# Kernel optimization log

Measured on AMD Instinct MI355X. Metric: run time of the kernel, lower is better.

## Reference

```python
import jax, jax.numpy as jnp
import numpy as np

# dims (see shape_source): seq S = d_t+1 must equal d_k for the unary quantum loader
B, T, D_IN = 128, 127, 48
DK = 128
S = T + 1            # tokens incl. class token; S == DK
H, L = 8, 6
P = (S * S - S) // 2  # RBS angles per head (pyramid circuit over S wires)


def _pyramid_pairs(n):
    # deterministic pyramid ordering of n(n-1)/2 adjacent-pair Givens rotations
    a, b = [], []
    for k in range(n - 1):
        for i in range(k, -1, -1):
            a.append(i)
            b.append(i + 1)
    return np.asarray(a, np.int32), np.asarray(b, np.int32)


def _build_W(phi, pa, pb, n):
    # classical simulation of the RBS pyramid circuit restricted to the unary
    # subspace: product of Givens rotations -> orthogonal n x n matrix
    def step(W, inp):
        ia, ib, th = inp
        c, s = jnp.cos(th), jnp.sin(th)
        ra, rb = W[ia], W[ib]
        W = W.at[ia].set(c * ra - s * rb)
        W = W.at[ib].set(s * ra + c * rb)
        return W, None
    W0 = jnp.eye(n, dtype=phi.dtype)
    W, _ = jax.lax.scan(step, W0, (pa, pb, phi))
    return W


def _layer_norm(x, g, b, eps=1e-5):
    m = jnp.mean(x, axis=-1, keepdims=True)
    v = jnp.mean((x - m) ** 2, axis=-1, keepdims=True)
    return (x - m) * jax.lax.rsqrt(v + eps) * g + b


def setup_inputs() -> dict:
    key = jax.random.key(0)
    ks = jax.random.split(key, 8)
    f32 = jnp.float32
    return {
        "x": jax.random.normal(ks[0], (B, T, D_IN), f32),
        "embed_w": jax.random.normal(ks[1], (DK, D_IN), f32) / np.sqrt(D_IN),
        "embed_b": jnp.zeros((DK,), f32),
        "class_token": jax.random.normal(ks[2], (DK,), f32) / DK,
        "norm0_g": jnp.ones((DK,), f32),
        "norm0_b": jnp.zeros((DK,), f32),
        "Vw": jax.random.normal(ks[3], (L, H, DK, DK), f32) / np.sqrt(DK),
        "Vb": jnp.zeros((L, H, DK), f32),
        "ln_g": jnp.ones((L, H, DK), f32),
        "ln_b": jnp.zeros((L, H, DK), f32),
        "phi": jax.random.normal(ks[4], (L, H, P), f32) / np.sqrt(S),
        "merger_w": jax.random.normal(ks[5], (L, H), f32) / np.sqrt(H),
        "merger_b": jnp.zeros((L,), f32),
    }


def reference(x, embed_w, embed_b, class_token, norm0_g, norm0_b,
              Vw, Vb, ln_g, ln_b, phi, merger_w, merger_b):
    Bsz = x.shape[0]
    pa, pb = _pyramid_pairs(S)
    # orthogonal score matrices for every (layer, head)
    Ws = jax.vmap(lambda p: _build_W(p, pa, pb, S))(phi.reshape(L * H, P))
    Ws = Ws.reshape(L, H, S, S)

    # embed patches, prepend class token (pos_embedding add is a no-op in the
    # original source: bare `+self.pos_embedding` statement, so it is omitted)
    tok = jnp.einsum('btf,df->btd', x, embed_w) + embed_b
    h = jnp.concatenate([jnp.broadcast_to(class_token, (Bsz, 1, DK)), tok], axis=1)
    h = _layer_norm(h, norm0_g, norm0_b)

    scale = 1.0 / np.sqrt(DK)
    for l in range(L):
        nrm = jnp.sqrt(jnp.sum(h * h, axis=-1))      # input3: token norms [B,S]
        u = h / nrm[..., None]                        # unit tokens (convert_array)
        hh, nn, uu = h, nrm, u

        def head(W, vw, vb, g, be):
            V = jnp.einsum('bsd,ed->bse', hh, vw) + vb
            M = jnp.einsum('bsd,de,bte->bst', uu, W, uu)
            A = (M * M) * (nn[:, :, None] * nn[:, None, :])
            Pm = jax.nn.softmax(A * scale, axis=-1)
            return _layer_norm(jnp.einsum('bst,btd->bsd', Pm, V) + hh, g, be)

        hs = jax.vmap(head)(Ws[l], Vw[l], Vb[l], ln_g[l], ln_b[l])  # [H,B,S,D]
        h = jnp.einsum('hbsd,h->bsd', hs, merger_w[l]) + merger_b[l]
    return h[:, -1, :]
```

## Files before the change

### kernel.cpp

```cpp
#include <hip/hip_runtime.h>
#include <hip/hip_bf16.h>


typedef __bf16 bf16x8 __attribute__((ext_vector_type(8)));
typedef float  f32x4  __attribute__((ext_vector_type(4)));
typedef unsigned int u32;
typedef u32 u32x4 __attribute__((ext_vector_type(4)));
typedef u32 u32x2 __attribute__((ext_vector_type(2)));
typedef unsigned short u16;

__device__ __forceinline__ int sidx(int row, int col)
{
    return row * 128 + ((((col >> 3) ^ (row & 15)) << 3) | (col & 7));
}

__device__ __forceinline__ void gll16(const void* g, void* l)
{
    __builtin_amdgcn_global_load_lds(
        (const __attribute__((address_space(1))) void*)g,
        (__attribute__((address_space(3))) void*)l, 16, 0, 0);
}

__global__ void __launch_bounds__(256)
prep_kernel(const float* __restrict__ phi, float2* __restrict__ csn,
            const float* __restrict__ vw,  __bf16* __restrict__ cvwf)
{
    if (blockIdx.x < 3072) {
        const int mat = blockIdx.x >> 6;
        const int t   = ((blockIdx.x & 63) << 2) + (threadIdx.x >> 6);
        const int j   = threadIdx.x & 63;
        float th = 0.f;
        if (t < 253) {
            const int p = t & 1, i = 2 * j + p;
            const int lim = min(t, 252 - t);
            if (i <= lim) {
                const int k = (t + i) >> 1;
                th = phi[mat * 8128 + ((k * (k + 1)) >> 1) + (k - i)];
            }
        }
        float sn, cs;
        __sincosf(th, &sn, &cs);
        csn[(mat * 256 + t) * 64 + j] = make_float2(cs, sn);
    } else {
        const int f    = (blockIdx.x - 3072) * 256 + threadIdx.x;
        const int lane = f & 63;
        const int k0   = (f >> 6) & 3;
        const int t    = (f >> 8) & 7;
        const int lh   = f >> 11;
        const int row  = t * 16 + (lane & 15);
        const int col  = k0 * 32 + (lane >> 4) * 8;
        const float* src = vw + (lh * 128 + row) * 128 + col;
        __bf16* dst = cvwf + f * 8;
#pragma unroll
        for (int j2 = 0; j2 < 8; j2++) dst[j2] = (__bf16)src[j2];
    }
}

__global__ void __launch_bounds__(64)
build_w_kernel(const float2* __restrict__ csn, __bf16* __restrict__ wt)
{
    const int mat = blockIdx.x >> 7;
    const int c0  = blockIdx.x & 127;
    const int lam = threadIdx.x;

    const float2* base = csn + (mat * 256) * 64 + lam;

    float vlo = (2 * lam     == c0) ? 1.f : 0.f;
    float vhi = (2 * lam + 1 == c0) ? 1.f : 0.f;

    float2 buf[3][16];
#pragma unroll
    for (int k = 0; k < 16; k++) buf[0][k] = base[k * 64];
#pragma unroll
    for (int k = 0; k < 16; k++) buf[1][k] = base[(16 + k) * 64];

#pragma unroll
    for (int g = 0; g < 16; g++) {
        const int cb = g % 3;
        if (g < 14) {
            const int nb = (g + 2) % 3;
#pragma unroll
            for (int k = 0; k < 16; k++)
                buf[nb][k] = base[((g + 2) * 16 + k) * 64];
        }
#pragma unroll
        for (int p = 0; p < 8; p++) {
            {
                const float cs = buf[cb][2 * p].x, sn = buf[cb][2 * p].y;
                float lo = vlo, hi = vhi;
                vlo = cs * lo - sn * hi;
                vhi = sn * lo + cs * hi;
            }
            {
                const float cs = buf[cb][2 * p + 1].x, sn = buf[cb][2 * p + 1].y;
                float y  = __shfl_down(vlo, 1);
                float x  = vhi;
                float xn = cs * x - sn * y;
                float yn = sn * x + cs * y;
                vhi = xn;
                float z = __shfl_up(yn, 1);
                if (lam > 0) vlo = z;
            }
        }
    }

    const int t    = c0 >> 4;
    const int k0w  = lam >> 4;
    const int quad = (lam >> 2) & 3;
    __bf16 va = (__bf16)vlo;
    __bf16 vb = (__bf16)vhi;
    u32 pk = (u32)__builtin_bit_cast(unsigned short, va)
           | ((u32)__builtin_bit_cast(unsigned short, vb) << 16);
    const int frag = (t * 4 + k0w) * 64 + quad * 16 + (c0 & 15);
    ((u32*)wt)[mat * 8192 + frag * 4 + (lam & 3)] = pk;
}

__global__ void __launch_bounds__(512)
embed_kernel(const float* __restrict__ x,  const float* __restrict__ ew,
             const float* __restrict__ eb, const float* __restrict__ ct,
             const float* __restrict__ g0, const float* __restrict__ b0,
             float* __restrict__ hf, __bf16* __restrict__ hb,
             float* __restrict__ invn)
{
    __shared__ float sx[4][48];
    __shared__ float sred[4][2];
    const int d  = threadIdx.x & 127, sq = threadIdx.x >> 7;
    const int wh = (threadIdx.x >> 6) & 1;
    const int b  = blockIdx.x & 127;
    const int s  = (blockIdx.x >> 7) * 4 + sq;

    if (s > 0 && d < 48) sx[sq][d] = x[(b * 127 + (s - 1)) * 48 + d];
    __syncthreads();

    float val;
    if (s == 0) {
        val = ct[d];
    } else {
        float aa = 0.f;
#pragma unroll
        for (int f = 0; f < 48; f++) aa = fmaf(sx[sq][f], ew[d * 48 + f], aa);
        val = aa + eb[d];
    }
    float v = val;
#pragma unroll
    for (int m = 32; m; m >>= 1) v += __shfl_xor(v, m);
    if ((threadIdx.x & 63) == 0) sred[sq][wh] = v;
    __syncthreads();
    float mean = (sred[sq][0] + sred[sq][1]) * (1.f / 128.f);
    float xc   = val - mean;
    __syncthreads();
    v = xc * xc;
#pragma unroll
    for (int m = 32; m; m >>= 1) v += __shfl_xor(v, m);
    if ((threadIdx.x & 63) == 0) sred[sq][wh] = v;
    __syncthreads();
    float var = (sred[sq][0] + sred[sq][1]) * (1.f / 128.f);
    float y   = xc * rsqrtf(var + 1e-5f) * g0[d] + b0[d];
    __syncthreads();
    v = y * y;
#pragma unroll
    for (int m = 32; m; m >>= 1) v += __shfl_xor(v, m);
    if ((threadIdx.x & 63) == 0) sred[sq][wh] = v;
    __syncthreads();
    float ss = sred[sq][0] + sred[sq][1];

    const int o = (b * 128 + s) * 128 + d;
    hf[o] = y;
    hb[o] = (__bf16)y;
    if (d == 0) invn[b * 128 + s] = rsqrtf(ss);
}

__global__ void __launch_bounds__(512, 4)
attn_kernel(int l, int last,
            const float*  __restrict__ hf,  const __bf16* __restrict__ hb,
            const float*  __restrict__ invn, const __bf16* __restrict__ wt,
            const __bf16* __restrict__ vwf, const float* __restrict__ vb,
            const float* __restrict__ lng,  const float* __restrict__ lnb,
            const float* __restrict__ mwp,  __bf16* __restrict__ hs)
{
    __shared__ __align__(16) __bf16 sH[128 * 128];
    __shared__ __align__(16) __bf16 sY[128 * 128];
    __shared__ float sInv[128];
    __shared__ float sVb[128];
    __shared__ float sLg[128];
    __shared__ float sLb[128];

    const int tid  = threadIdx.x;
    const int lane = tid & 63, w = tid >> 6;
    const int l15  = lane & 15, quad = lane >> 4;
    const int b    = blockIdx.x & 127;
    const int hh   = blockIdx.x >> 7;
    const int lh   = l * 8 + hh;

    const __bf16* hbp   = hb  + b * 16384;
    const __bf16* wbase = wt  + (size_t)lh * 16384;
    const __bf16* vbase = vwf + (size_t)lh * 16384;

#pragma unroll
    for (int c = 0; c < 4; c++) {
        const int ch  = tid + c * 512;
        const int row = ch >> 4, cc = ch & 15;
        const int sc  = cc ^ (row & 15);
        gll16(hbp + (row * 16 + sc) * 8, &sH[(c * 512 + w * 64) * 8]);
    }
    if (tid < 128) {
        sInv[tid] = invn[b * 128 + tid];
        sVb[tid]  = vb[lh * 128 + tid];
        sLg[tid]  = lng[lh * 128 + tid];
        sLb[tid]  = lnb[lh * 128 + tid];
    }
    __syncthreads();

    const int r0 = w * 16;
    const int kq = quad * 8;
    const int q4 = quad * 4;
    const f32x4 vzero = {0.f, 0.f, 0.f, 0.f};
    const bool active = !last || (w == 7);

    f32x4 acc[8];

    auto mmGA = [&](const __bf16* gB) {
#pragma unroll
        for (int t = 0; t < 8; t++) acc[t] = vzero;
        __builtin_amdgcn_s_setprio(1);
#pragma unroll
        for (int k0c = 0; k0c < 4; k0c++) {
            bf16x8 a0 = *(const bf16x8*)(&sH[sidx(r0 + l15, k0c * 32 + kq)]);
#pragma unroll
            for (int t = 0; t < 8; t++) {
                bf16x8 bb = *(const bf16x8*)(gB + ((t * 4 + k0c) * 64 + lane) * 8);
                acc[t] = __builtin_amdgcn_mfma_f32_16x16x32_bf16(a0, bb, acc[t], 0, 0, 0);
            }
        }
        __builtin_amdgcn_s_setprio(0);
    };

    auto mmLL = [&](const __bf16* Ab, const __bf16* Bb) {
#pragma unroll
        for (int t = 0; t < 8; t++) acc[t] = vzero;
        __builtin_amdgcn_s_setprio(1);
#pragma unroll
        for (int k0 = 0; k0 < 128; k0 += 32) {
            const int kk = k0 + kq;
            bf16x8 a0 = *(const bf16x8*)(&Ab[sidx(r0 + l15, kk)]);
#pragma unroll
            for (int t = 0; t < 8; t++) {
                bf16x8 bb = *(const bf16x8*)(&Bb[sidx(t * 16 + l15, kk)]);
                acc[t] = __builtin_amdgcn_mfma_f32_16x16x32_bf16(a0, bb, acc[t], 0, 0, 0);
            }
        }
        __builtin_amdgcn_s_setprio(0);
    };

    float hres[8][4];

    if (active) {
        mmGA(wbase);
#pragma unroll
        for (int t = 0; t < 8; t++)
#pragma unroll
            for (int r = 0; r < 4; r++)
                sY[sidx(r0 + q4 + r, t * 16 + l15)] = (__bf16)acc[t][r];

        mmLL(sY, sH);

        {
            const float scale2 = 0.08838834764831843f * 1.4426950408889634f;
            float invt[8];
#pragma unroll
            for (int t = 0; t < 8; t++) invt[t] = sInv[t * 16 + l15];
            float invs[4];
#pragma unroll
            for (int r = 0; r < 4; r++) invs[r] = sInv[r0 + q4 + r];

            float mx[4] = {-3e38f, -3e38f, -3e38f, -3e38f};
#pragma unroll
            for (int t = 0; t < 8; t++)
#pragma unroll
                for (int r = 0; r < 4; r++) {
                    float g = acc[t][r];
                    float v = g * g * invs[r] * invt[t] * scale2;
                    acc[t][r] = v;
                    mx[r] = fmaxf(mx[r], v);
                }
#pragma unroll
            for (int m = 1; m < 16; m <<= 1)
#pragma unroll
                for (int r = 0; r < 4; r++) mx[r] = fmaxf(mx[r], __shfl_xor(mx[r], m));

            float sm[4] = {0.f, 0.f, 0.f, 0.f};
#pragma unroll
            for (int t = 0; t < 8; t++)
#pragma unroll
                for (int r = 0; r < 4; r++) {
                    float e = exp2f(acc[t][r] - mx[r]);
                    acc[t][r] = e;
                    sm[r] += e;
                }
#pragma unroll
            for (int m = 1; m < 16; m <<= 1)
#pragma unroll
                for (int r = 0; r < 4; r++) sm[r] += __shfl_xor(sm[r], m);
#pragma unroll
            for (int r = 0; r < 4; r++) sm[r] = 1.0f / sm[r];
#pragma unroll
            for (int t = 0; t < 8; t++)
#pragma unroll
                for (int r = 0; r < 4; r++)
                    sY[sidx(r0 + q4 + r, t * 16 + l15)] = (__bf16)(acc[t][r] * sm[r]);
        }

        {
            const float* hfp = hf + (b * 128 + r0 + q4) * 128;
#pragma unroll
            for (int t = 0; t < 8; t++)
#pragma unroll
                for (int r = 0; r < 4; r++)
                    hres[t][r] = hfp[r * 128 + t * 16 + l15];
        }
    }

    mmGA(vbase);
    __syncthreads();

    {
#pragma unroll
        for (int t = 0; t < 8; t++) {
            const float vbv = sVb[t * 16 + l15];
            __bf16 b0 = (__bf16)(acc[t][0] + vbv);
            __bf16 b1 = (__bf16)(acc[t][1] + vbv);
            __bf16 b2 = (__bf16)(acc[t][2] + vbv);
            __bf16 b3 = (__bf16)(acc[t][3] + vbv);
            u32 w0 = (u32)__builtin_bit_cast(u16, b0)
                   | ((u32)__builtin_bit_cast(u16, b1) << 16);
            u32 w1 = (u32)__builtin_bit_cast(u16, b2)
                   | ((u32)__builtin_bit_cast(u16, b3) << 16);
            u32x2 pv = {w0, w1};
            *(u32x2*)(&sH[sidx(t * 16 + l15, r0 + q4)]) = pv;
        }
    }
    __syncthreads();

    if (active) {
        mmLL(sY, sH);

        {
            const float mw = mwp[lh];
            float lgv[8], lbv[8];
#pragma unroll
            for (int t = 0; t < 8; t++) {
                lgv[t] = sLg[t * 16 + l15];
                lbv[t] = sLb[t * 16 + l15];
            }
            float sum_[4] = {0.f, 0.f, 0.f, 0.f};
            float sq_[4]  = {0.f, 0.f, 0.f, 0.f};
#pragma unroll
            for (int t = 0; t < 8; t++)
#pragma unroll
                for (int r = 0; r < 4; r++) {
                    float xx = acc[t][r] + hres[t][r];
                    acc[t][r] = xx;
                    sum_[r] += xx;
                    sq_[r]  += xx * xx;
                }
#pragma unroll
            for (int m = 1; m < 16; m <<= 1)
#pragma unroll
                for (int r = 0; r < 4; r++) {
                    sum_[r] += __shfl_xor(sum_[r], m);
                    sq_[r]  += __shfl_xor(sq_[r], m);
                }
            float mean[4], rstd[4];
#pragma unroll
            for (int r = 0; r < 4; r++) {
                mean[r] = sum_[r] * (1.f / 128.f);
                float var = sq_[r] * (1.f / 128.f) - mean[r] * mean[r];
                rstd[r] = rsqrtf(fmaxf(var, 0.f) + 1e-5f);
            }
            __bf16* hsp = hs + ((hh * 128 + b) * 128 + r0 + q4) * 128;
#pragma unroll
            for (int t = 0; t < 8; t++)
#pragma unroll
                for (int r = 0; r < 4; r++) {
                    if (!last || (q4 + r == 15)) {
                        float y = (acc[t][r] - mean[r]) * rstd[r] * lgv[t] + lbv[t];
                        hsp[r * 128 + t * 16 + l15] = (__bf16)(y * mw);
                    }
                }
        }
    }
}

__global__ void __launch_bounds__(256)
merge_kernel(const __bf16* __restrict__ hs, const float* __restrict__ mbp, int l,
             float* __restrict__ hf, __bf16* __restrict__ hb, float* __restrict__ invn,
             float* __restrict__ out, int last)
{
    const int lane = threadIdx.x & 63;
    const int wv   = threadIdx.x >> 6;
    const int sq   = lane >> 4;
    const int dl   = lane & 15;
    const int d0   = dl * 8;
    const float mbv = mbp[l];

    int b, s;
    if (last) {
        b = blockIdx.x * 16 + wv * 4 + sq;
        s = 127;
    } else {
        b = blockIdx.x & 127;
        s = (blockIdx.x >> 7) * 16 + wv * 4 + sq;
    }

    float a[8];
#pragma unroll
    for (int j = 0; j < 8; j++) a[j] = mbv;
#pragma unroll
    for (int h8 = 0; h8 < 8; h8++) {
        bf16x8 v = *(const bf16x8*)(hs + (((size_t)h8 * 128 + b) * 128 + s) * 128 + d0);
#pragma unroll
        for (int j = 0; j < 8; j++) a[j] += (float)v[j];
    }

    if (last) {
        float4 f0 = {a[0], a[1], a[2], a[3]};
        float4 f1 = {a[4], a[5], a[6], a[7]};
        *(float4*)(out + b * 128 + d0)     = f0;
        *(float4*)(out + b * 128 + d0 + 4) = f1;
        return;
    }

    float ss = 0.f;
#pragma unroll
    for (int j = 0; j < 8; j++) ss = fmaf(a[j], a[j], ss);
#pragma unroll
    for (int m = 1; m < 16; m <<= 1) ss += __shfl_xor(ss, m);

    const size_t o = ((size_t)b * 128 + s) * 128 + d0;
    float4 f0 = {a[0], a[1], a[2], a[3]};
    float4 f1 = {a[4], a[5], a[6], a[7]};
    *(float4*)(hf + o)     = f0;
    *(float4*)(hf + o + 4) = f1;

    u32 pk[4];
#pragma unroll
    for (int j2 = 0; j2 < 4; j2++) {
        __bf16 x0 = (__bf16)a[2 * j2], x1 = (__bf16)a[2 * j2 + 1];
        pk[j2] = (u32)__builtin_bit_cast(unsigned short, x0)
               | ((u32)__builtin_bit_cast(unsigned short, x1) << 16);
    }
    u32x4 pv = {pk[0], pk[1], pk[2], pk[3]};
    *(u32x4*)(hb + o) = pv;

    if (dl == 0) invn[b * 128 + s] = rsqrtf(ss);
}

extern "C" void kernel_launch(void* const* d_in, const int* in_sizes, int n_in,
                              void* d_out, int out_size, void* d_ws, size_t ws_size,
                              hipStream_t stream)
{
    (void)in_sizes; (void)n_in; (void)out_size; (void)ws_size;

    const float* x   = (const float*)d_in[0];
    const float* ew  = (const float*)d_in[1];
    const float* eb  = (const float*)d_in[2];
    const float* ct  = (const float*)d_in[3];
    const float* g0  = (const float*)d_in[4];
    const float* b0  = (const float*)d_in[5];
    const float* vw  = (const float*)d_in[6];
    const float* vb  = (const float*)d_in[7];
    const float* lng = (const float*)d_in[8];
    const float* lnb = (const float*)d_in[9];
    const float* phi = (const float*)d_in[10];
    const float* mw  = (const float*)d_in[11];
    const float* mb  = (const float*)d_in[12];
    float* out = (float*)d_out;

    char* ws = (char*)d_ws;
    __bf16* wt   = (__bf16*)(ws);
    float*  hf   = (float*)(ws + 1572864);
    __bf16* hb   = (__bf16*)(ws + 9961472);
    float*  invn = (float*)(ws + 14155776);
    __bf16* hs   = (__bf16*)(ws + 14221312);
    __bf16* cvwf = (__bf16*)(ws + 47775744);
    float2* csn  = (float2*)(ws + 49348608);

    prep_kernel<<<3456, 256, 0, stream>>>(phi, csn, vw, cvwf);
    build_w_kernel<<<6144, 64, 0, stream>>>(csn, wt);
    embed_kernel<<<4096, 512, 0, stream>>>(x, ew, eb, ct, g0, b0, hf, hb, invn);
    for (int l = 0; l < 6; l++) {
        const int last = (l == 5) ? 1 : 0;
        attn_kernel<<<1024, 512, 0, stream>>>(l, last, hf, hb, invn, wt, cvwf,
                                              vb, lng, lnb, mw, hs);
        merge_kernel<<<last ? 8 : 1024, 256, 0, stream>>>(hs, mb, l, hf, hb,
                                                          invn, out, last);
    }
}
```

Baseline: 425.7 us.

## Share Givens coefficients across four columns via double-buffered LDS in build_w

```diff
diff --git a/kernel.cpp b/kernel.cpp
--- a/kernel.cpp
+++ b/kernel.cpp
@@ -56,43 +56,46 @@
     }
 }
 
-__global__ void __launch_bounds__(64)
+__global__ void __launch_bounds__(256)
 build_w_kernel(const float2* __restrict__ csn, __bf16* __restrict__ wt)
 {
-    const int mat = blockIdx.x >> 7;
-    const int c0  = blockIdx.x & 127;
-    const int lam = threadIdx.x;
-
-    const float2* base = csn + (mat * 256) * 64 + lam;
-
-    float vlo = (2 * lam     == c0) ? 1.f : 0.f;
-    float vhi = (2 * lam + 1 == c0) ? 1.f : 0.f;
-
-    float2 buf[3][16];
-#pragma unroll
-    for (int k = 0; k < 16; k++) buf[0][k] = base[k * 64];
-#pragma unroll
-    for (int k = 0; k < 16; k++) buf[1][k] = base[(16 + k) * 64];
-
-#pragma unroll
-    for (int g = 0; g < 16; g++) {
-        const int cb = g % 3;
-        if (g < 14) {
-            const int nb = (g + 2) % 3;
-#pragma unroll
-            for (int k = 0; k < 16; k++)
-                buf[nb][k] = base[((g + 2) * 16 + k) * 64];
-        }
+    __shared__ __align__(16) float2 scsn[2][16][64];
+
+    const int tid = threadIdx.x;
+    const int lam = tid & 63;
+    const int wv  = tid >> 6;
+    const int mat = blockIdx.x >> 5;
+    const int col = (blockIdx.x & 31) * 4 + wv;
+
+    const char* csnm = (const char*)(csn + (size_t)mat * 256 * 64);
+
+    gll16(csnm + tid * 16,        (char*)scsn[0] + tid * 16);
+    gll16(csnm + 4096 + tid * 16, (char*)scsn[0] + 4096 + tid * 16);
+
+    float vlo = (2 * lam     == col) ? 1.f : 0.f;
+    float vhi = (2 * lam + 1 == col) ? 1.f : 0.f;
+    __syncthreads();
+
+    for (int g = 0; g < 16; ++g) {
+        if (g < 15) {
+            const char* srcg = csnm + (size_t)(g + 1) * 8192;
+            char* dstg = (char*)scsn[(g + 1) & 1];
+            gll16(srcg + tid * 16,        dstg + tid * 16);
+            gll16(srcg + 4096 + tid * 16, dstg + 4096 + tid * 16);
+        }
+        float2 lb[16];
+#pragma unroll
+        for (int k = 0; k < 16; k++) lb[k] = scsn[g & 1][k][lam];
 #pragma unroll
         for (int p = 0; p < 8; p++) {
             {
-                const float cs = buf[cb][2 * p].x, sn = buf[cb][2 * p].y;
+                const float cs = lb[2 * p].x, sn = lb[2 * p].y;
                 float lo = vlo, hi = vhi;
                 vlo = cs * lo - sn * hi;
                 vhi = sn * lo + cs * hi;
             }
             {
-                const float cs = buf[cb][2 * p + 1].x, sn = buf[cb][2 * p + 1].y;
+                const float cs = lb[2 * p + 1].x, sn = lb[2 * p + 1].y;
                 float y  = __shfl_down(vlo, 1);
                 float x  = vhi;
                 float xn = cs * x - sn * y;
@@ -102,16 +105,17 @@
                 if (lam > 0) vlo = z;
             }
         }
-    }
-
-    const int t    = c0 >> 4;
+        __syncthreads();
+    }
+
+    const int t    = col >> 4;
     const int k0w  = lam >> 4;
     const int quad = (lam >> 2) & 3;
     __bf16 va = (__bf16)vlo;
     __bf16 vb = (__bf16)vhi;
     u32 pk = (u32)__builtin_bit_cast(unsigned short, va)
            | ((u32)__builtin_bit_cast(unsigned short, vb) << 16);
-    const int frag = (t * 4 + k0w) * 64 + quad * 16 + (c0 & 15);
+    const int frag = (t * 4 + k0w) * 64 + quad * 16 + (col & 15);
     ((u32*)wt)[mat * 8192 + frag * 4 + (lam & 3)] = pk;
 }
 
@@ -486,7 +490,7 @@
     float2* csn  = (float2*)(ws + 49348608);
 
     prep_kernel<<<3456, 256, 0, stream>>>(phi, csn, vw, cvwf);
-    build_w_kernel<<<6144, 64, 0, stream>>>(csn, wt);
+    build_w_kernel<<<1536, 256, 0, stream>>>(csn, wt);
     embed_kernel<<<4096, 512, 0, stream>>>(x, ew, eb, ct, g0, b0, hf, hb, invn);
     for (int l = 0; l < 6; l++) {
         const int last = (l == 5) ? 1 : 0;
```

New measurement: 414.1 us (median of 2 runs). 2.7% less time.
